# Kernel tuning notes

Hardware: AMD Instinct MI355X
Metric: run time of the kernel (lower is better)

The kernel has to match this reference:

```python
import jax, jax.numpy as jnp
import numpy as np

EPS = 1e-20
K = 3        # kernel_size
STRIDE = 1
PAD = 1
DIL = 1


def kernel_channels(x):
    # torch.nn.Unfold-style rolling: (B,C,H,W) -> (B,C,K*K,H_out,W_out)
    B, C, H, W = x.shape
    xp = jnp.pad(x, ((0, 0), (0, 0), (PAD, PAD), (PAD, PAD)))
    Hp, Wp = H + 2 * PAD, W + 2 * PAD
    H_out = (Hp - DIL * (K - 1) - 1) // STRIDE + 1
    W_out = (Wp - DIL * (K - 1) - 1) // STRIDE + 1
    patches = [
        xp[:, :,
           i * DIL:i * DIL + (H_out - 1) * STRIDE + 1:STRIDE,
           j * DIL:j * DIL + (W_out - 1) * STRIDE + 1:STRIDE]
        for i in range(K) for j in range(K)
    ]
    return jnp.stack(patches, axis=2)


def setup_inputs() -> dict:
    key = jax.random.key(0)
    ks = jax.random.split(key, 7)
    B, C, H, W = 4, 16, 256, 256
    d = jax.random.normal(ks[0], (B, C, H, W), dtype=jnp.float32)
    cd = jax.random.uniform(ks[1], (B, C, H, W), dtype=jnp.float32)
    s = jax.random.uniform(ks[2], (B, C, H, W), dtype=jnp.float32)
    cs = jax.random.uniform(ks[3], (B, C, H, W), dtype=jnp.float32)
    s_prod_roll = jax.random.uniform(ks[4], (B, C, K * K, H, W), dtype=jnp.float32)
    # nconv enforces non-negative weights (softplus in enforce_limits)
    spatial_weight = jax.nn.softplus(
        jax.random.normal(ks[5], (C, 1, K * K, 1, 1), dtype=jnp.float32))
    channel_weight = jax.nn.softplus(
        jax.random.normal(ks[6], (C, C, 1, 1), dtype=jnp.float32))
    return {"d": d, "cd": cd, "s": s, "cs": cs, "s_prod_roll": s_prod_roll,
            "spatial_weight": spatial_weight, "channel_weight": channel_weight}


def reference(d, cd, s, cs, s_prod_roll, spatial_weight, channel_weight):
    devalue_conf = 1.0 / (STRIDE * STRIDE)
    d_roll = kernel_channels(d)          # B,C,K*K,H',W'
    cd_roll = kernel_channels(cd)
    cd_prop = cd_roll * s_prod_roll

    sw = spatial_weight[:, 0, :, 0, 0]   # (C, K*K) — grouped conv3d == per-channel weighted sum
    nom = jnp.einsum('bckhw,ck->bchw', cd_prop * d_roll, sw)
    denom = jnp.einsum('bckhw,ck->bchw', cd_prop, sw)
    d_spatial = nom / (denom + EPS)
    cd_spatial = denom / (jnp.sum(spatial_weight) + EPS)

    cw = channel_weight[:, :, 0, 0]      # (O, C) — 1x1 conv
    nom2 = jnp.einsum('bchw,oc->bohw', cd_spatial * d_spatial, cw)
    denom2 = jnp.einsum('bchw,oc->bohw', cd_spatial, cw)
    d_out = nom2 / (denom2 + EPS)
    cd_out = denom2 / (jnp.sum(channel_weight) + EPS)
    return (d_out, cd_out * devalue_conf)
```

## Files before the change

kernel.cpp:

```cpp
#include <hip/hip_runtime.h>


#define NB 4
#define NC 16
#define NH 256
#define NW 256
#define NK 9
#define HW (NH * NW)
#define TPB 64

static constexpr float kEPS = 1e-20f;

__device__ __forceinline__ float frcp(float x) { return __builtin_amdgcn_rcpf(x); }

__global__ __launch_bounds__(TPB) void structnconv_fused(
    const float* __restrict__ g_d,
    const float* __restrict__ g_cd,
    const float* __restrict__ g_sp,
    const float* __restrict__ g_sw,
    const float* __restrict__ g_cw,
    float* __restrict__ g_dout,
    float* __restrict__ g_cdout)
{
    __shared__ float lds_pd[NC][NW];
    __shared__ float lds_cs[NC][NW];
    __shared__ float lds_sw[NC * NK];
    __shared__ float lds_cw[NC * NC];

    const int t = threadIdx.x;

    const float a0 = g_sw[t], a1 = g_sw[64 + t];
    const float a2 = (t < NC * NK - 128) ? g_sw[128 + t] : 0.f;
    lds_sw[t] = a0;
    lds_sw[64 + t] = a1;
    if (t < NC * NK - 128) lds_sw[128 + t] = a2;
    const float c0 = g_cw[t], c1 = g_cw[64 + t], c2 = g_cw[128 + t], c3 = g_cw[192 + t];
    lds_cw[t] = c0; lds_cw[64 + t] = c1; lds_cw[128 + t] = c2; lds_cw[192 + t] = c3;
    float s1 = a0 + a1 + a2;
    float s2 = c0 + c1 + c2 + c3;
    #pragma unroll
    for (int off = 32; off > 0; off >>= 1) {
        s1 += __shfl_down(s1, off);
        s2 += __shfl_down(s2, off);
    }
    const float inv_sw_sum = frcp(__shfl(s1, 0) + kEPS);
    const float inv_cw_sum = frcp(__shfl(s2, 0) + kEPS);

    const int bid = (int)blockIdx.x;
    const int swz = (bid & 7) * 128 + (bid >> 3);
    const int b = swz >> 8;
    const int h = swz & (NH - 1);
    const int w0 = t << 2;
    const int pix = h * NW + w0;

    #pragma unroll 1
    for (int c = 0; c < NC; ++c) {
        const float* pdd = g_d  + (size_t)(b * NC + c) * HW + pix;
        const float* pcc = g_cd + (size_t)(b * NC + c) * HW + pix;
        const float* pss = g_sp + ((size_t)(b * NC + c) * NK) * HW + pix;

        float dr[3][6], cr[3][6];
        #pragma unroll
        for (int r = 0; r < 3; ++r) {
            const int hh = h + r - 1;
            const int roff = (r - 1) * NW;
            if ((unsigned)hh < (unsigned)NH) {
                const float4 md = *(const float4*)(pdd + roff);
                const float4 mc = *(const float4*)(pcc + roff);
                dr[r][1] = md.x; dr[r][2] = md.y; dr[r][3] = md.z; dr[r][4] = md.w;
                cr[r][1] = mc.x; cr[r][2] = mc.y; cr[r][3] = mc.z; cr[r][4] = mc.w;
                dr[r][0] = (w0 > 0)       ? pdd[roff - 1] : 0.f;
                cr[r][0] = (w0 > 0)       ? pcc[roff - 1] : 0.f;
                dr[r][5] = (w0 + 4 < NW)  ? pdd[roff + 4] : 0.f;
                cr[r][5] = (w0 + 4 < NW)  ? pcc[roff + 4] : 0.f;
            } else {
                #pragma unroll
                for (int j = 0; j < 6; ++j) { dr[r][j] = 0.f; cr[r][j] = 0.f; }
            }
        }

        float4 sp[NK];
        #pragma unroll
        for (int k = 0; k < NK; ++k)
            sp[k] = *(const float4*)(pss + (size_t)k * HW);

        float nom[4] = {0.f, 0.f, 0.f, 0.f};
        float den[4] = {0.f, 0.f, 0.f, 0.f};
        #pragma unroll
        for (int r = 0; r < 3; ++r) {
            #pragma unroll
            for (int dj = 0; dj < 3; ++dj) {
                const int k = r * 3 + dj;
                const float wck = lds_sw[c * NK + k];
                const float sv[4] = {sp[k].x, sp[k].y, sp[k].z, sp[k].w};
                #pragma unroll
                for (int p = 0; p < 4; ++p) {
                    const float cdp = cr[r][dj + p] * sv[p];
                    nom[p] = fmaf(cdp * dr[r][dj + p], wck, nom[p]);
                    den[p] = fmaf(cdp, wck, den[p]);
                }
            }
        }

        float4 csv, pdv;
        csv.x = den[0] * inv_sw_sum;  pdv.x = csv.x * (nom[0] * frcp(den[0] + kEPS));
        csv.y = den[1] * inv_sw_sum;  pdv.y = csv.y * (nom[1] * frcp(den[1] + kEPS));
        csv.z = den[2] * inv_sw_sum;  pdv.z = csv.z * (nom[2] * frcp(den[2] + kEPS));
        csv.w = den[3] * inv_sw_sum;  pdv.w = csv.w * (nom[3] * frcp(den[3] + kEPS));
        *(float4*)&lds_cs[c][w0] = csv;
        *(float4*)&lds_pd[c][w0] = pdv;
    }

    const size_t outb = (size_t)b * NC * HW + pix;
    #pragma unroll 1
    for (int oc = 0; oc < 4; ++oc) {
        float4 an[4], ad[4];
        #pragma unroll
        for (int o4 = 0; o4 < 4; ++o4) {
            an[o4] = make_float4(0.f, 0.f, 0.f, 0.f);
            ad[o4] = make_float4(0.f, 0.f, 0.f, 0.f);
        }
        #pragma unroll
        for (int c = 0; c < NC; ++c) {
            const float4 pdv = *(const float4*)&lds_pd[c][w0];
            const float4 csv = *(const float4*)&lds_cs[c][w0];
            #pragma unroll
            for (int o4 = 0; o4 < 4; ++o4) {
                const float wv = lds_cw[(oc * 4 + o4) * NC + c];
                an[o4].x = fmaf(pdv.x, wv, an[o4].x);
                an[o4].y = fmaf(pdv.y, wv, an[o4].y);
                an[o4].z = fmaf(pdv.z, wv, an[o4].z);
                an[o4].w = fmaf(pdv.w, wv, an[o4].w);
                ad[o4].x = fmaf(csv.x, wv, ad[o4].x);
                ad[o4].y = fmaf(csv.y, wv, ad[o4].y);
                ad[o4].z = fmaf(csv.z, wv, ad[o4].z);
                ad[o4].w = fmaf(csv.w, wv, ad[o4].w);
            }
        }
        #pragma unroll
        for (int o4 = 0; o4 < 4; ++o4) {
            const int o = oc * 4 + o4;
            float4 dv, cv;
            dv.x = an[o4].x * frcp(ad[o4].x + kEPS);
            dv.y = an[o4].y * frcp(ad[o4].y + kEPS);
            dv.z = an[o4].z * frcp(ad[o4].z + kEPS);
            dv.w = an[o4].w * frcp(ad[o4].w + kEPS);
            cv.x = ad[o4].x * inv_cw_sum;
            cv.y = ad[o4].y * inv_cw_sum;
            cv.z = ad[o4].z * inv_cw_sum;
            cv.w = ad[o4].w * inv_cw_sum;
            *(float4*)(g_dout  + outb + (size_t)o * HW) = dv;
            *(float4*)(g_cdout + outb + (size_t)o * HW) = cv;
        }
    }
}

extern "C" void kernel_launch(void* const* d_in, const int* in_sizes, int n_in,
                              void* d_out, int out_size, void* d_ws, size_t ws_size,
                              hipStream_t stream) {
    const float* g_d  = (const float*)d_in[0];
    const float* g_cd = (const float*)d_in[1];
    const float* g_sp = (const float*)d_in[4];
    const float* g_sw = (const float*)d_in[5];
    const float* g_cw = (const float*)d_in[6];

    float* g_dout  = (float*)d_out;
    float* g_cdout = g_dout + (size_t)NB * NC * HW;

    const int blocks = NB * NH;
    structnconv_fused<<<blocks, TPB, 0, stream>>>(g_d, g_cd, g_sp, g_sw, g_cw,
                                                  g_dout, g_cdout);
}
```

Baseline: 41.20 us.

## Split input channels across two waves with register accumulation and LDS reduction

Each block now runs two waves that each handle half of the input channels for the same row. Every wave folds its channel contributions straight into per-output register accumulators instead of staging all intermediates in LDS. The two partial sums are then exchanged through a smaller LDS buffer, and each wave finishes and stores half of the output channels. This doubles per-row parallelism and memory-level parallelism, at the cost of a larger register footprint (128 accumulator floats) and an extra block-wide barrier.

```diff
diff --git a/kernel.cpp b/kernel.cpp
--- a/kernel.cpp
+++ b/kernel.cpp
@@ -7,7 +7,7 @@
 #define NW 256
 #define NK 9
 #define HW (NH * NW)
-#define TPB 64
+#define TPB 128
 
 static constexpr float kEPS = 1e-20f;
 
@@ -22,39 +22,55 @@
     float* __restrict__ g_dout,
     float* __restrict__ g_cdout)
 {
-    __shared__ float lds_pd[NC][NW];
-    __shared__ float lds_cs[NC][NW];
     __shared__ float lds_sw[NC * NK];
     __shared__ float lds_cw[NC * NC];
+    __shared__ float lds_part[4];
+    __shared__ float lds_x[2][8][2][NW];
 
-    const int t = threadIdx.x;
+    const int t  = threadIdx.x;
+    const int wv = t >> 6;
+    const int ln = t & 63;
 
-    const float a0 = g_sw[t], a1 = g_sw[64 + t];
-    const float a2 = (t < NC * NK - 128) ? g_sw[128 + t] : 0.f;
-    lds_sw[t] = a0;
-    lds_sw[64 + t] = a1;
-    if (t < NC * NK - 128) lds_sw[128 + t] = a2;
-    const float c0 = g_cw[t], c1 = g_cw[64 + t], c2 = g_cw[128 + t], c3 = g_cw[192 + t];
-    lds_cw[t] = c0; lds_cw[64 + t] = c1; lds_cw[128 + t] = c2; lds_cw[192 + t] = c3;
-    float s1 = a0 + a1 + a2;
-    float s2 = c0 + c1 + c2 + c3;
+    float s1 = g_sw[t];
+    float s2 = g_cw[t] + g_cw[TPB + t];
+    lds_sw[t] = s1;
+    lds_cw[t] = g_cw[t];
+    lds_cw[TPB + t] = g_cw[TPB + t];
+    if (t < NC * NK - TPB) {
+        const float v = g_sw[TPB + t];
+        lds_sw[TPB + t] = v;
+        s1 += v;
+    }
     #pragma unroll
     for (int off = 32; off > 0; off >>= 1) {
         s1 += __shfl_down(s1, off);
         s2 += __shfl_down(s2, off);
     }
-    const float inv_sw_sum = frcp(__shfl(s1, 0) + kEPS);
-    const float inv_cw_sum = frcp(__shfl(s2, 0) + kEPS);
+    if (ln == 0) {
+        lds_part[wv]     = s1;
+        lds_part[2 + wv] = s2;
+    }
+    __syncthreads();
+    const float inv_sw_sum = frcp(lds_part[0] + lds_part[1] + kEPS);
+    const float inv_cw_sum = frcp(lds_part[2] + lds_part[3] + kEPS);
 
     const int bid = (int)blockIdx.x;
     const int swz = (bid & 7) * 128 + (bid >> 3);
     const int b = swz >> 8;
     const int h = swz & (NH - 1);
-    const int w0 = t << 2;
+    const int w0 = ln << 2;
     const int pix = h * NW + w0;
 
+    float4 an[NC], ad[NC];
+    #pragma unroll
+    for (int o = 0; o < NC; ++o) {
+        an[o] = make_float4(0.f, 0.f, 0.f, 0.f);
+        ad[o] = make_float4(0.f, 0.f, 0.f, 0.f);
+    }
+
     #pragma unroll 1
-    for (int c = 0; c < NC; ++c) {
+    for (int ci = 0; ci < 8; ++ci) {
+        const int c = (wv << 3) + ci;
         const float* pdd = g_d  + (size_t)(b * NC + c) * HW + pix;
         const float* pcc = g_cd + (size_t)(b * NC + c) * HW + pix;
         const float* pss = g_sp + ((size_t)(b * NC + c) * NK) * HW + pix;
@@ -69,10 +85,10 @@
                 const float4 mc = *(const float4*)(pcc + roff);
                 dr[r][1] = md.x; dr[r][2] = md.y; dr[r][3] = md.z; dr[r][4] = md.w;
                 cr[r][1] = mc.x; cr[r][2] = mc.y; cr[r][3] = mc.z; cr[r][4] = mc.w;
-                dr[r][0] = (w0 > 0)       ? pdd[roff - 1] : 0.f;
-                cr[r][0] = (w0 > 0)       ? pcc[roff - 1] : 0.f;
-                dr[r][5] = (w0 + 4 < NW)  ? pdd[roff + 4] : 0.f;
-                cr[r][5] = (w0 + 4 < NW)  ? pcc[roff + 4] : 0.f;
+                dr[r][0] = (w0 > 0)      ? pdd[roff - 1] : 0.f;
+                cr[r][0] = (w0 > 0)      ? pcc[roff - 1] : 0.f;
+                dr[r][5] = (w0 + 4 < NW) ? pdd[roff + 4] : 0.f;
+                cr[r][5] = (w0 + 4 < NW) ? pcc[roff + 4] : 0.f;
             } else {
                 #pragma unroll
                 for (int j = 0; j < 6; ++j) { dr[r][j] = 0.f; cr[r][j] = 0.f; }
@@ -107,52 +123,53 @@
         csv.y = den[1] * inv_sw_sum;  pdv.y = csv.y * (nom[1] * frcp(den[1] + kEPS));
         csv.z = den[2] * inv_sw_sum;  pdv.z = csv.z * (nom[2] * frcp(den[2] + kEPS));
         csv.w = den[3] * inv_sw_sum;  pdv.w = csv.w * (nom[3] * frcp(den[3] + kEPS));
-        *(float4*)&lds_cs[c][w0] = csv;
-        *(float4*)&lds_pd[c][w0] = pdv;
+
+        #pragma unroll
+        for (int o = 0; o < NC; ++o) {
+            const float wcv = lds_cw[o * NC + c];
+            an[o].x = fmaf(pdv.x, wcv, an[o].x);
+            an[o].y = fmaf(pdv.y, wcv, an[o].y);
+            an[o].z = fmaf(pdv.z, wcv, an[o].z);
+            an[o].w = fmaf(pdv.w, wcv, an[o].w);
+            ad[o].x = fmaf(csv.x, wcv, ad[o].x);
+            ad[o].y = fmaf(csv.y, wcv, ad[o].y);
+            ad[o].z = fmaf(csv.z, wcv, ad[o].z);
+            ad[o].w = fmaf(csv.w, wcv, ad[o].w);
+        }
     }
 
+    #define XWRITE(BASE)                                                   \
+        _Pragma("unroll")                                                  \
+        for (int ol = 0; ol < 8; ++ol) {                                   \
+            *(float4*)&lds_x[wv][ol][0][w0] = an[(BASE) + ol];             \
+            *(float4*)&lds_x[wv][ol][1][w0] = ad[(BASE) + ol];             \
+        }
+    if (wv == 0) { XWRITE(8) } else { XWRITE(0) }
+    #undef XWRITE
+
+    __syncthreads();
+
     const size_t outb = (size_t)b * NC * HW + pix;
-    #pragma unroll 1
-    for (int oc = 0; oc < 4; ++oc) {
-        float4 an[4], ad[4];
-        #pragma unroll
-        for (int o4 = 0; o4 < 4; ++o4) {
-            an[o4] = make_float4(0.f, 0.f, 0.f, 0.f);
-            ad[o4] = make_float4(0.f, 0.f, 0.f, 0.f);
+    #define FINISH(BASE)                                                   \
+        _Pragma("unroll")                                                  \
+        for (int ol = 0; ol < 8; ++ol) {                                   \
+            const int o = (BASE) + ol;                                     \
+            const float4 xn = *(const float4*)&lds_x[wv ^ 1][ol][0][w0];   \
+            const float4 xd = *(const float4*)&lds_x[wv ^ 1][ol][1][w0];   \
+            const float nx = an[o].x + xn.x, dx = ad[o].x + xd.x;          \
+            const float ny = an[o].y + xn.y, dy = ad[o].y + xd.y;          \
+            const float nz = an[o].z + xn.z, dz = ad[o].z + xd.z;          \
+            const float nw_ = an[o].w + xn.w, dw = ad[o].w + xd.w;         \
+            float4 dv, cv;                                                 \
+            dv.x = nx * frcp(dx + kEPS);  cv.x = dx * inv_cw_sum;          \
+            dv.y = ny * frcp(dy + kEPS);  cv.y = dy * inv_cw_sum;          \
+            dv.z = nz * frcp(dz + kEPS);  cv.z = dz * inv_cw_sum;          \
+            dv.w = nw_ * frcp(dw + kEPS); cv.w = dw * inv_cw_sum;          \
+            *(float4*)(g_dout  + outb + (size_t)o * HW) = dv;              \
+            *(float4*)(g_cdout + outb + (size_t)o * HW) = cv;              \
         }
-        #pragma unroll
-        for (int c = 0; c < NC; ++c) {
-            const float4 pdv = *(const float4*)&lds_pd[c][w0];
-            const float4 csv = *(const float4*)&lds_cs[c][w0];
-            #pragma unroll
-            for (int o4 = 0; o4 < 4; ++o4) {
-                const float wv = lds_cw[(oc * 4 + o4) * NC + c];
-                an[o4].x = fmaf(pdv.x, wv, an[o4].x);
-                an[o4].y = fmaf(pdv.y, wv, an[o4].y);
-                an[o4].z = fmaf(pdv.z, wv, an[o4].z);
-                an[o4].w = fmaf(pdv.w, wv, an[o4].w);
-                ad[o4].x = fmaf(csv.x, wv, ad[o4].x);
-                ad[o4].y = fmaf(csv.y, wv, ad[o4].y);
-                ad[o4].z = fmaf(csv.z, wv, ad[o4].z);
-                ad[o4].w = fmaf(csv.w, wv, ad[o4].w);
-            }
-        }
-        #pragma unroll
-        for (int o4 = 0; o4 < 4; ++o4) {
-            const int o = oc * 4 + o4;
-            float4 dv, cv;
-            dv.x = an[o4].x * frcp(ad[o4].x + kEPS);
-            dv.y = an[o4].y * frcp(ad[o4].y + kEPS);
-            dv.z = an[o4].z * frcp(ad[o4].z + kEPS);
-            dv.w = an[o4].w * frcp(ad[o4].w + kEPS);
-            cv.x = ad[o4].x * inv_cw_sum;
-            cv.y = ad[o4].y * inv_cw_sum;
-            cv.z = ad[o4].z * inv_cw_sum;
-            cv.w = ad[o4].w * inv_cw_sum;
-            *(float4*)(g_dout  + outb + (size_t)o * HW) = dv;
-            *(float4*)(g_cdout + outb + (size_t)o * HW) = cv;
-        }
-    }
+    if (wv == 0) { FINISH(0) } else { FINISH(8) }
+    #undef FINISH
 }
 
 extern "C" void kernel_launch(void* const* d_in, const int* in_sizes, int n_in,
```

Measured after the change: 38.01 us. -7.7%, faster.

## Split channel and output loops across four wavefronts per block

Applied to the files above, without the earlier changes.

Each block grows from one wavefront to four. Each wavefront handles four input channels in the spatial stage and four output channels in the 1x1 channel-mix stage, with a block barrier between the stages and a cross-wave reduction for the weight sums. The goal is to shorten the serial per-thread channel loops and expose more memory-level parallelism per row. The costs are the extra __syncthreads and a 32KB LDS footprint per block, which may limit how many blocks fit on each CU.

```diff
diff --git a/kernel.cpp b/kernel.cpp
--- a/kernel.cpp
+++ b/kernel.cpp
@@ -7,13 +7,13 @@
 #define NW 256
 #define NK 9
 #define HW (NH * NW)
-#define TPB 64
+#define TPB 256
 
 static constexpr float kEPS = 1e-20f;
 
 __device__ __forceinline__ float frcp(float x) { return __builtin_amdgcn_rcpf(x); }
 
-__global__ __launch_bounds__(TPB) void structnconv_fused(
+__global__ __launch_bounds__(TPB, 4) void structnconv_fused(
     const float* __restrict__ g_d,
     const float* __restrict__ g_cd,
     const float* __restrict__ g_sp,
@@ -22,39 +22,44 @@
     float* __restrict__ g_dout,
     float* __restrict__ g_cdout)
 {
-    __shared__ float lds_pd[NC][NW];
-    __shared__ float lds_cs[NC][NW];
+    __shared__ float lds_sp[NC][2][NW];
     __shared__ float lds_sw[NC * NK];
     __shared__ float lds_cw[NC * NC];
+    __shared__ float lds_part[8];
 
-    const int t = threadIdx.x;
+    const int t  = threadIdx.x;
+    const int wv = t >> 6;
+    const int ln = t & 63;
 
-    const float a0 = g_sw[t], a1 = g_sw[64 + t];
-    const float a2 = (t < NC * NK - 128) ? g_sw[128 + t] : 0.f;
-    lds_sw[t] = a0;
-    lds_sw[64 + t] = a1;
-    if (t < NC * NK - 128) lds_sw[128 + t] = a2;
-    const float c0 = g_cw[t], c1 = g_cw[64 + t], c2 = g_cw[128 + t], c3 = g_cw[192 + t];
-    lds_cw[t] = c0; lds_cw[64 + t] = c1; lds_cw[128 + t] = c2; lds_cw[192 + t] = c3;
-    float s1 = a0 + a1 + a2;
-    float s2 = c0 + c1 + c2 + c3;
+    float s1 = (t < NC * NK) ? g_sw[t] : 0.f;
+    float s2 = g_cw[t];
+    if (t < NC * NK) lds_sw[t] = s1;
+    lds_cw[t] = s2;
     #pragma unroll
     for (int off = 32; off > 0; off >>= 1) {
         s1 += __shfl_down(s1, off);
         s2 += __shfl_down(s2, off);
     }
-    const float inv_sw_sum = frcp(__shfl(s1, 0) + kEPS);
-    const float inv_cw_sum = frcp(__shfl(s2, 0) + kEPS);
+    if (ln == 0) {
+        lds_part[wv]     = s1;
+        lds_part[4 + wv] = s2;
+    }
+    __syncthreads();
+    const float inv_sw_sum =
+        frcp(lds_part[0] + lds_part[1] + lds_part[2] + lds_part[3] + kEPS);
+    const float inv_cw_sum =
+        frcp(lds_part[4] + lds_part[5] + lds_part[6] + lds_part[7] + kEPS);
 
     const int bid = (int)blockIdx.x;
     const int swz = (bid & 7) * 128 + (bid >> 3);
     const int b = swz >> 8;
     const int h = swz & (NH - 1);
-    const int w0 = t << 2;
+    const int w0 = ln << 2;
     const int pix = h * NW + w0;
 
     #pragma unroll 1
-    for (int c = 0; c < NC; ++c) {
+    for (int ci = 0; ci < 4; ++ci) {
+        const int c = (wv << 2) + ci;
         const float* pdd = g_d  + (size_t)(b * NC + c) * HW + pix;
         const float* pcc = g_cd + (size_t)(b * NC + c) * HW + pix;
         const float* pss = g_sp + ((size_t)(b * NC + c) * NK) * HW + pix;
@@ -69,10 +74,10 @@
                 const float4 mc = *(const float4*)(pcc + roff);
                 dr[r][1] = md.x; dr[r][2] = md.y; dr[r][3] = md.z; dr[r][4] = md.w;
                 cr[r][1] = mc.x; cr[r][2] = mc.y; cr[r][3] = mc.z; cr[r][4] = mc.w;
-                dr[r][0] = (w0 > 0)       ? pdd[roff - 1] : 0.f;
-                cr[r][0] = (w0 > 0)       ? pcc[roff - 1] : 0.f;
-                dr[r][5] = (w0 + 4 < NW)  ? pdd[roff + 4] : 0.f;
-                cr[r][5] = (w0 + 4 < NW)  ? pcc[roff + 4] : 0.f;
+                dr[r][0] = (w0 > 0)      ? pdd[roff - 1] : 0.f;
+                cr[r][0] = (w0 > 0)      ? pcc[roff - 1] : 0.f;
+                dr[r][5] = (w0 + 4 < NW) ? pdd[roff + 4] : 0.f;
+                cr[r][5] = (w0 + 4 < NW) ? pcc[roff + 4] : 0.f;
             } else {
                 #pragma unroll
                 for (int j = 0; j < 6; ++j) { dr[r][j] = 0.f; cr[r][j] = 0.f; }
@@ -107,51 +112,52 @@
         csv.y = den[1] * inv_sw_sum;  pdv.y = csv.y * (nom[1] * frcp(den[1] + kEPS));
         csv.z = den[2] * inv_sw_sum;  pdv.z = csv.z * (nom[2] * frcp(den[2] + kEPS));
         csv.w = den[3] * inv_sw_sum;  pdv.w = csv.w * (nom[3] * frcp(den[3] + kEPS));
-        *(float4*)&lds_cs[c][w0] = csv;
-        *(float4*)&lds_pd[c][w0] = pdv;
+        *(float4*)&lds_sp[c][0][w0] = pdv;
+        *(float4*)&lds_sp[c][1][w0] = csv;
+    }
+
+    __syncthreads();
+
+    const int o_base = wv << 2;
+    float4 an[4], ad[4];
+    #pragma unroll
+    for (int ol = 0; ol < 4; ++ol) {
+        an[ol] = make_float4(0.f, 0.f, 0.f, 0.f);
+        ad[ol] = make_float4(0.f, 0.f, 0.f, 0.f);
+    }
+    #pragma unroll
+    for (int c = 0; c < NC; ++c) {
+        const float4 pdv = *(const float4*)&lds_sp[c][0][w0];
+        const float4 csv = *(const float4*)&lds_sp[c][1][w0];
+        #pragma unroll
+        for (int ol = 0; ol < 4; ++ol) {
+            const float wcv = lds_cw[(o_base + ol) * NC + c];
+            an[ol].x = fmaf(pdv.x, wcv, an[ol].x);
+            an[ol].y = fmaf(pdv.y, wcv, an[ol].y);
+            an[ol].z = fmaf(pdv.z, wcv, an[ol].z);
+            an[ol].w = fmaf(pdv.w, wcv, an[ol].w);
+            ad[ol].x = fmaf(csv.x, wcv, ad[ol].x);
+            ad[ol].y = fmaf(csv.y, wcv, ad[ol].y);
+            ad[ol].z = fmaf(csv.z, wcv, ad[ol].z);
+            ad[ol].w = fmaf(csv.w, wcv, ad[ol].w);
+        }
     }
 
     const size_t outb = (size_t)b * NC * HW + pix;
-    #pragma unroll 1
-    for (int oc = 0; oc < 4; ++oc) {
-        float4 an[4], ad[4];
-        #pragma unroll
-        for (int o4 = 0; o4 < 4; ++o4) {
-            an[o4] = make_float4(0.f, 0.f, 0.f, 0.f);
-            ad[o4] = make_float4(0.f, 0.f, 0.f, 0.f);
-        }
-        #pragma unroll
-        for (int c = 0; c < NC; ++c) {
-            const float4 pdv = *(const float4*)&lds_pd[c][w0];
-            const float4 csv = *(const float4*)&lds_cs[c][w0];
-            #pragma unroll
-            for (int o4 = 0; o4 < 4; ++o4) {
-                const float wv = lds_cw[(oc * 4 + o4) * NC + c];
-                an[o4].x = fmaf(pdv.x, wv, an[o4].x);
-                an[o4].y = fmaf(pdv.y, wv, an[o4].y);
-                an[o4].z = fmaf(pdv.z, wv, an[o4].z);
-                an[o4].w = fmaf(pdv.w, wv, an[o4].w);
-                ad[o4].x = fmaf(csv.x, wv, ad[o4].x);
-                ad[o4].y = fmaf(csv.y, wv, ad[o4].y);
-                ad[o4].z = fmaf(csv.z, wv, ad[o4].z);
-                ad[o4].w = fmaf(csv.w, wv, ad[o4].w);
-            }
-        }
-        #pragma unroll
-        for (int o4 = 0; o4 < 4; ++o4) {
-            const int o = oc * 4 + o4;
-            float4 dv, cv;
-            dv.x = an[o4].x * frcp(ad[o4].x + kEPS);
-            dv.y = an[o4].y * frcp(ad[o4].y + kEPS);
-            dv.z = an[o4].z * frcp(ad[o4].z + kEPS);
-            dv.w = an[o4].w * frcp(ad[o4].w + kEPS);
-            cv.x = ad[o4].x * inv_cw_sum;
-            cv.y = ad[o4].y * inv_cw_sum;
-            cv.z = ad[o4].z * inv_cw_sum;
-            cv.w = ad[o4].w * inv_cw_sum;
-            *(float4*)(g_dout  + outb + (size_t)o * HW) = dv;
-            *(float4*)(g_cdout + outb + (size_t)o * HW) = cv;
-        }
+    #pragma unroll
+    for (int ol = 0; ol < 4; ++ol) {
+        const int o = o_base + ol;
+        float4 dv, cv;
+        dv.x = an[ol].x * frcp(ad[ol].x + kEPS);
+        dv.y = an[ol].y * frcp(ad[ol].y + kEPS);
+        dv.z = an[ol].z * frcp(ad[ol].z + kEPS);
+        dv.w = an[ol].w * frcp(ad[ol].w + kEPS);
+        cv.x = ad[ol].x * inv_cw_sum;
+        cv.y = ad[ol].y * inv_cw_sum;
+        cv.z = ad[ol].z * inv_cw_sum;
+        cv.w = ad[ol].w * inv_cw_sum;
+        *(float4*)(g_dout  + outb + (size_t)o * HW) = dv;
+        *(float4*)(g_cdout + outb + (size_t)o * HW) = cv;
     }
 }
 
```

Result: slower. 49.59 us (+20.4%).
